# Performance work log

Hardware: AMD Instinct MI355X
Metric: run time of the kernel (lower is better)

## Reference

```python
import jax, jax.numpy as jnp
import numpy as np

N_DIMS = 8
MAPPING_DIMS = [0, 2, 4, 6]
COND_DIMS = [1, 3, 5, 7]
N_BINS = 32
MIN_BIN_W = 1e-3
MIN_BIN_H = 1e-3
MIN_DERIV = 1e-3
PI = np.pi
N = 524288


def _gather(v, idx):
    # v: (..., K[+1]), idx: (...) -> (...)
    return jnp.take_along_axis(v, idx[..., None], axis=-1)[..., 0]


def circular_quadratic_spline(x, uw, uh, ud, inverse):
    """Circular rational-quadratic spline on [-pi, pi] (Durkan et al. / Rezende et al.).
    x: (N, M); uw, uh, ud: (N, M, K)."""
    K = uw.shape[-1]
    left, right, bottom, top = -PI, PI, -PI, PI
    # circular boundary: derivative at right edge == derivative at left edge
    ud = jnp.concatenate([ud, ud[..., :1]], axis=-1)  # (N, M, K+1)

    widths = jax.nn.softmax(uw, axis=-1)
    widths = MIN_BIN_W + (1.0 - MIN_BIN_W * K) * widths
    cumw = jnp.pad(jnp.cumsum(widths, axis=-1), [(0, 0), (0, 0), (1, 0)])
    cumw = left + (right - left) * cumw
    cumw = cumw.at[..., 0].set(left).at[..., -1].set(right)
    widths = cumw[..., 1:] - cumw[..., :-1]

    derivatives = MIN_DERIV + jax.nn.softplus(ud)

    heights = jax.nn.softmax(uh, axis=-1)
    heights = MIN_BIN_H + (1.0 - MIN_BIN_H * K) * heights
    cumh = jnp.pad(jnp.cumsum(heights, axis=-1), [(0, 0), (0, 0), (1, 0)])
    cumh = bottom + (top - bottom) * cumh
    cumh = cumh.at[..., 0].set(bottom).at[..., -1].set(top)
    heights = cumh[..., 1:] - cumh[..., :-1]

    # per-element bin search (searchsorted via comparison-sum)
    bins = cumh if inverse else cumw
    idx = jnp.clip(jnp.sum(x[..., None] >= bins, axis=-1) - 1, 0, K - 1)

    in_cumw = _gather(cumw, idx)
    in_w = _gather(widths, idx)
    in_cumh = _gather(cumh, idx)
    in_delta = _gather(heights / widths, idx)
    d0 = _gather(derivatives, idx)
    d1 = _gather(derivatives, idx + 1)
    in_h = _gather(heights, idx)

    if inverse:
        dy = x - in_cumh
        s = d0 + d1 - 2.0 * in_delta
        a = dy * s + in_h * (in_delta - d0)
        b = in_h * d0 - dy * s
        c_ = -in_delta * dy
        disc = b * b - 4.0 * a * c_
        root = (2.0 * c_) / (-b - jnp.sqrt(disc))
        out = root * in_w + in_cumw
        t1m = root * (1.0 - root)
        denom = in_delta + s * t1m
        dnum = in_delta ** 2 * (d1 * root ** 2 + 2.0 * in_delta * t1m + d0 * (1.0 - root) ** 2)
        logabsdet = -(jnp.log(dnum) - 2.0 * jnp.log(denom))
        return out, logabsdet
    theta = (x - in_cumw) / in_w
    t1m = theta * (1.0 - theta)
    s = d0 + d1 - 2.0 * in_delta
    denom = in_delta + s * t1m
    num = in_h * (in_delta * theta ** 2 + d0 * t1m)
    out = in_cumh + num / denom
    dnum = in_delta ** 2 * (d1 * theta ** 2 + 2.0 * in_delta * t1m + d0 * (1.0 - theta) ** 2)
    logabsdet = jnp.log(dnum) - 2.0 * jnp.log(denom)
    return out, logabsdet


def setup_inputs() -> dict:
    key = jax.random.key(0)
    ks = jax.random.split(key, 8)
    x = jax.random.uniform(ks[0], (N, N_DIMS), jnp.float32, minval=-PI, maxval=PI)
    c = jax.random.normal(ks[1], (N, 128), jnp.float32)
    W1 = jax.random.normal(ks[2], (256, 140), jnp.float32) * (140 ** -0.5)
    b1 = jax.random.normal(ks[3], (256,), jnp.float32) * 0.01
    W2 = jax.random.normal(ks[4], (256, 256), jnp.float32) * (256 ** -0.5)
    b2 = jax.random.normal(ks[5], (256,), jnp.float32) * 0.01
    W3 = jax.random.normal(ks[6], (384, 256), jnp.float32) * (256 ** -0.5)
    b3 = jax.random.normal(ks[7], (384,), jnp.float32) * 0.01
    return {"x": x, "c": c, "W1": W1, "b1": b1, "W2": W2, "b2": b2,
            "W3": W3, "b3": b3, "inverse": 0}


def reference(x, c, W1, b1, W2, b2, W3, b3, inverse):
    m_idx = jnp.array(MAPPING_DIMS)
    c_idx = jnp.array(COND_DIMS)
    x_map = x[..., m_idx]          # (N, 4)
    x_cond = x[..., c_idx]         # (N, 4)
    inp = jnp.concatenate([x_cond, jnp.sin(x_cond), jnp.cos(x_cond), c], axis=-1)
    h = jax.nn.leaky_relu(inp @ W1.T + b1, negative_slope=0.01)
    h = jax.nn.leaky_relu(h @ W2.T + b2, negative_slope=0.01)
    outs = (h @ W3.T + b3).reshape(x.shape[0], len(MAPPING_DIMS), N_BINS, 3)
    w, hh, d = outs[..., 0], outs[..., 1], outs[..., 2]
    y_map, logabsdet = circular_quadratic_spline(x_map, w, hh, d, bool(inverse))
    y_unsort = jnp.concatenate([y_map, x_cond], axis=-1)
    perm = [0] * N_DIMS
    for i, j in enumerate(MAPPING_DIMS + COND_DIMS):
        perm[j] = i
    y = y_unsort[..., jnp.array(perm)]
    return y, logabsdet.sum(axis=-1)
```

## Files before the change

kernel.cpp:

```cpp
#include <hip/hip_runtime.h>
#include <math.h>

#define NROWS_TOTAL 524288
#define BR 64
#define NTH 512
#define PI_F 3.14159265358979323846f
#define TWO_PI_F 6.28318530717958647692f

typedef float f32x4 __attribute__((ext_vector_type(4)));
typedef _Float16 half8 __attribute__((ext_vector_type(8)));
typedef _Float16 half4v __attribute__((ext_vector_type(4)));

#define OFF_A 0
#define OFF_B 67584
#define LDS_BYTES 135168
#define PITCH_ACT 528
#define PITCH_OUT 1540
#define OFF_LAD 100352

#define W1_OFF 0
#define W2_OFF 40960
#define W3_OFF 106496
#define WHI_TOT 204800

struct h2 { _Float16 hi, lo; };
__device__ __forceinline__ h2 split16(float v){
  h2 r;
  r.hi = (_Float16)v;
  r.lo = (_Float16)(v - (float)r.hi);
  return r;
}

template<int NK, int NCT, bool RELU, bool OUTF32>
__device__ __forceinline__ void gemm_phase(unsigned char* LDS,
    const _Float16* __restrict__ WH, const _Float16* __restrict__ WL,
    const float* __restrict__ bias,
    int srcOff, int dstOff, int wave, int lrow, int lhi)
{
  constexpr int NS = NK / 32;
  f32x4 acc[4][NCT];
  #pragma unroll
  for (int rg = 0; rg < 4; rg++)
    #pragma unroll
    for (int ct = 0; ct < NCT; ct++)
      acc[rg][ct] = (f32x4){0.f, 0.f, 0.f, 0.f};

  const int ko = lhi * 8;
  #pragma unroll
  for (int ksl = 0; ksl < NS; ksl++){
    half8 ah[4], al[4];
    #pragma unroll
    for (int rg = 0; rg < 4; rg++){
      const unsigned char* p = LDS + srcOff + (rg * 16 + lrow) * PITCH_ACT
                               + (ksl * 32 + ko) * 2;
      ah[rg] = *(const half8*)p;
      al[rg] = *(const half8*)(p + 64 * PITCH_ACT);
    }
    #pragma unroll
    for (int ct = 0; ct < NCT; ct++){
      const int o = (wave * NCT + ct) * 16 + lrow;
      const size_t woff = (size_t)o * NK + ksl * 32 + ko;
      half8 wh = *(const half8*)(WH + woff);
      half8 wl = *(const half8*)(WL + woff);
      #pragma unroll
      for (int rg = 0; rg < 4; rg++){
        acc[rg][ct] = __builtin_amdgcn_mfma_f32_16x16x32_f16(ah[rg], wh, acc[rg][ct], 0, 0, 0);
        acc[rg][ct] = __builtin_amdgcn_mfma_f32_16x16x32_f16(al[rg], wh, acc[rg][ct], 0, 0, 0);
        acc[rg][ct] = __builtin_amdgcn_mfma_f32_16x16x32_f16(ah[rg], wl, acc[rg][ct], 0, 0, 0);
      }
    }
  }
  __syncthreads();
  #pragma unroll
  for (int ct = 0; ct < NCT; ct++){
    const int col = (wave * NCT + ct) * 16 + lrow;
    const float bv = bias[col];
    #pragma unroll
    for (int rg = 0; rg < 4; rg++){
      #pragma unroll
      for (int j = 0; j < 4; j++){
        float v = acc[rg][ct][j] + bv;
        if (RELU) v = (v >= 0.f) ? v : 0.01f * v;
        const int row = rg * 16 + lhi * 4 + j;
        if (OUTF32){
          *(float*)(LDS + (size_t)row * PITCH_OUT + col * 4) = v;
        } else {
          h2 s = split16(v);
          *(_Float16*)(LDS + dstOff + row * PITCH_ACT + col * 2) = s.hi;
          *(_Float16*)(LDS + dstOff + (row + 64) * PITCH_ACT + col * 2) = s.lo;
        }
      }
    }
  }
  __syncthreads();
}

__global__ void wconv_kernel(const float* __restrict__ W1, const float* __restrict__ W2,
                             const float* __restrict__ W3, _Float16* __restrict__ wb)
{
  int i = blockIdx.x * 256 + threadIdx.x;
  float v;
  if (i < 40960){
    int o = i / 160, k = i - o * 160;
    v = (k < 140) ? W1[o * 140 + k] : 0.f;
  } else if (i < 106496){
    v = W2[i - 40960];
  } else {
    v = W3[i - 106496];
  }
  h2 s = split16(v);
  wb[i] = s.hi;
  wb[i + WHI_TOT] = s.lo;
}

__global__ __launch_bounds__(NTH, 2) void spline_fused(
    const float* __restrict__ x, const float* __restrict__ c,
    const float* __restrict__ b1, const float* __restrict__ b2,
    const float* __restrict__ b3, const _Float16* __restrict__ wb,
    const int* __restrict__ invp, float* __restrict__ out)
{
  __shared__ __align__(16) unsigned char LDS[LDS_BYTES];
  const int tid  = threadIdx.x;
  const int wave = tid >> 6;
  const int lane = tid & 63;
  const int lrow = lane & 15;
  const int lhi  = lane >> 4;
  const int row0 = blockIdx.x * BR;

  {
    const float4* c4 = (const float4*)(c + (size_t)row0 * 128);
    #pragma unroll
    for (int i = 0; i < 4; i++){
      int q = tid + i * NTH;
      float4 v = c4[q];
      int r = q >> 5, cg = (q & 31) * 4 + 12;
      h2 s0 = split16(v.x), s1 = split16(v.y), s2 = split16(v.z), s3 = split16(v.w);
      half4v hv = {s0.hi, s1.hi, s2.hi, s3.hi};
      half4v lv = {s0.lo, s1.lo, s2.lo, s3.lo};
      *(half4v*)(LDS + OFF_B + r * PITCH_ACT + cg * 2) = hv;
      *(half4v*)(LDS + OFF_B + (r + 64) * PITCH_ACT + cg * 2) = lv;
    }
    if (tid < BR){
      int n = row0 + tid;
      float4 xa = *(const float4*)(x + (size_t)n * 8);
      float4 xb = *(const float4*)(x + (size_t)n * 8 + 4);
      float xc0 = xa.y, xc1 = xa.w, xc2 = xb.y, xc3 = xb.w;
      float f[12] = {xc0, xc1, xc2, xc3,
                     sinf(xc0), sinf(xc1), sinf(xc2), sinf(xc3),
                     cosf(xc0), cosf(xc1), cosf(xc2), cosf(xc3)};
      unsigned char* rp = LDS + OFF_B + tid * PITCH_ACT;
      #pragma unroll
      for (int g = 0; g < 3; g++){
        h2 s0 = split16(f[4*g+0]), s1 = split16(f[4*g+1]);
        h2 s2 = split16(f[4*g+2]), s3 = split16(f[4*g+3]);
        half4v hv = {s0.hi, s1.hi, s2.hi, s3.hi};
        half4v lv = {s0.lo, s1.lo, s2.lo, s3.lo};
        *(half4v*)(rp + g * 8) = hv;
        *(half4v*)(rp + 64 * PITCH_ACT + g * 8) = lv;
      }
      #pragma unroll
      for (int z = 0; z < 5; z++){
        *(unsigned long long*)(rp + 280 + z * 8) = 0ull;
        *(unsigned long long*)(rp + 64 * PITCH_ACT + 280 + z * 8) = 0ull;
      }
    }
  }
  __syncthreads();

  const _Float16* WLO = wb + WHI_TOT;
  gemm_phase<160, 2, true , false>(LDS, wb + W1_OFF, WLO + W1_OFF, b1, OFF_B, OFF_A, wave, lrow, lhi);
  gemm_phase<256, 2, true , false>(LDS, wb + W2_OFF, WLO + W2_OFF, b2, OFF_A, OFF_B, wave, lrow, lhi);
  gemm_phase<256, 3, false, true >(LDS, wb + W3_OFF, WLO + W3_OFF, b3, OFF_B, 0,     wave, lrow, lhi);

  if (tid < 256){
    const int r = tid & 63;
    const int d = tid >> 6;
    const int n = row0 + r;
    const int inv = invp[0];

    const float* ob = (const float*)(LDS + (size_t)r * PITCH_OUT) + d * 96;

    float wn[32], hn[32];
    float mw = ob[0], mh = ob[1];
    #pragma unroll
    for (int b = 1; b < 32; b++){
      mw = fmaxf(mw, ob[3*b]);
      mh = fmaxf(mh, ob[3*b + 1]);
    }
    float sw = 0.f, sh = 0.f;
    #pragma unroll
    for (int b = 0; b < 32; b++){
      float ew = expf(ob[3*b] - mw);     wn[b] = ew; sw += ew;
      float eh = expf(ob[3*b + 1] - mh); hn[b] = eh; sh += eh;
    }
    const float C1 = 1.0f - 32.0f * 1e-3f;
    float iw = C1 / sw, ih = C1 / sh;
    #pragma unroll
    for (int b = 0; b < 32; b++){
      wn[b] = 1e-3f + wn[b] * iw;
      hn[b] = 1e-3f + hn[b] * ih;
    }

    float2 xv = *(const float2*)(x + (size_t)n * 8 + 2 * d);
    float xm = xv.x, xcv = xv.y;

    bool fnd = false; int idx = 31;
    float cw = -PI_F, loA = 0.f, szA = 0.f;
    #pragma unroll
    for (int b = 0; b < 31; b++){
      float wbv = TWO_PI_F * (inv ? hn[b] : wn[b]);
      float reb = cw + wbv;
      if (!fnd && xm < reb){ fnd = true; idx = b; loA = cw; szA = wbv; }
      cw = reb;
    }
    if (!fnd){ loA = cw; szA = PI_F - cw; }

    float ch = -PI_F, loB = 0.f, szB = 0.f;
    #pragma unroll
    for (int b = 0; b < 31; b++){
      float hbv = TWO_PI_F * (inv ? wn[b] : hn[b]);
      if (b == idx){ loB = ch; szB = hbv; }
      ch += hbv;
    }
    if (idx == 31){ loB = ch; szB = PI_F - ch; }

    float le, wbw, lh, hb;
    if (inv){ lh = loA; hb = szA; le = loB; wbw = szB; }
    else    { le = loA; wbw = szA; lh = loB; hb = szB; }

    int i2 = (idx + 1) & 31;
    float ud0 = ob[idx * 3 + 2];
    float ud1 = ob[i2  * 3 + 2];
    auto softplus = [](float v) -> float {
      return fmaxf(v, 0.f) + log1pf(expf(-fabsf(v)));
    };
    float d0 = 1e-3f + softplus(ud0);
    float d1 = 1e-3f + softplus(ud1);

    float delta = hb / wbw;
    float outv, lad;
    if (inv){
      float dy = xm - lh;
      float s  = d0 + d1 - 2.f * delta;
      float aq = dy * s + hb * (delta - d0);
      float bq = hb * d0 - dy * s;
      float cq = -delta * dy;
      float disc = bq * bq - 4.f * aq * cq;
      float root = (2.f * cq) / (-bq - sqrtf(disc));
      outv = root * wbw + le;
      float t1m = root * (1.f - root);
      float denom = delta + s * t1m;
      float dnum = delta * delta * (d1 * root * root + 2.f * delta * t1m + d0 * (1.f - root) * (1.f - root));
      lad = -(logf(dnum) - 2.f * logf(denom));
    } else {
      float theta = (xm - le) / wbw;
      float t1m = theta * (1.f - theta);
      float s   = d0 + d1 - 2.f * delta;
      float denom = delta + s * t1m;
      float num = hb * (delta * theta * theta + d0 * t1m);
      outv = lh + num / denom;
      float dnum = delta * delta * (d1 * theta * theta + 2.f * delta * t1m + d0 * (1.f - theta) * (1.f - theta));
      lad = logf(dnum) - 2.f * logf(denom);
    }

    out[(size_t)n * 8 + 2 * d]     = outv;
    out[(size_t)n * 8 + 2 * d + 1] = xcv;
    *(float*)(LDS + OFF_LAD + (r * 4 + d) * 4) = lad;
  }
  __syncthreads();
  if (tid < BR){
    const float* lp = (const float*)(LDS + OFF_LAD);
    float sld = lp[tid * 4] + lp[tid * 4 + 1] + lp[tid * 4 + 2] + lp[tid * 4 + 3];
    out[(size_t)NROWS_TOTAL * 8 + row0 + tid] = sld;
  }
}

extern "C" void kernel_launch(void* const* d_in, const int* in_sizes, int n_in,
                              void* d_out, int out_size, void* d_ws, size_t ws_size,
                              hipStream_t stream)
{
  (void)in_sizes; (void)n_in; (void)out_size; (void)ws_size;
  const float* x  = (const float*)d_in[0];
  const float* c  = (const float*)d_in[1];
  const float* W1 = (const float*)d_in[2];
  const float* b1 = (const float*)d_in[3];
  const float* W2 = (const float*)d_in[4];
  const float* b2 = (const float*)d_in[5];
  const float* W3 = (const float*)d_in[6];
  const float* b3 = (const float*)d_in[7];
  const int*  inv = (const int*)d_in[8];
  _Float16* wb = (_Float16*)d_ws;
  float* out = (float*)d_out;

  hipLaunchKernelGGL(wconv_kernel, dim3(800), dim3(256), 0, stream, W1, W2, W3, wb);
  hipLaunchKernelGGL(spline_fused, dim3(NROWS_TOTAL / BR), dim3(NTH), 0, stream,
                     x, c, b1, b2, b3, wb, inv, out);
}
```

Before: 1.300 ms.

## Shrink LDS to a single activation buffer and split spline epilogue for higher occupancy

The kernel now keeps one in-place activation buffer, holding GEMM results in registers across a barrier before overwriting it, which halves LDS use. The f32 logits are staged in two 32-row halves so they fit, and the spline runs on 128 threads per half. Launch bounds rise to 4 blocks per CU to exploit the smaller footprint, and weight fragments are double-buffered across k-slices to hide global load latency. Risks include register pressure under the tighter occupancy bound, extra barriers, and a spline stage with less parallelism per half.

```diff
diff --git a/kernel.cpp b/kernel.cpp
--- a/kernel.cpp
+++ b/kernel.cpp
@@ -11,12 +11,10 @@
 typedef _Float16 half8 __attribute__((ext_vector_type(8)));
 typedef _Float16 half4v __attribute__((ext_vector_type(4)));
 
-#define OFF_A 0
-#define OFF_B 67584
-#define LDS_BYTES 135168
 #define PITCH_ACT 528
 #define PITCH_OUT 1540
-#define OFF_LAD 100352
+#define OFF_LAD 67584
+#define LDS_BYTES 68608
 
 #define W1_OFF 0
 #define W2_OFF 40960
@@ -31,14 +29,13 @@
   return r;
 }
 
-template<int NK, int NCT, bool RELU, bool OUTF32>
-__device__ __forceinline__ void gemm_phase(unsigned char* LDS,
+template<int NK, int NCT>
+__device__ __forceinline__ void gemm_core(const unsigned char* LDS,
+    f32x4 (&acc)[4][NCT],
     const _Float16* __restrict__ WH, const _Float16* __restrict__ WL,
-    const float* __restrict__ bias,
-    int srcOff, int dstOff, int wave, int lrow, int lhi)
+    int wave, int lrow, int lhi)
 {
   constexpr int NS = NK / 32;
-  f32x4 acc[4][NCT];
   #pragma unroll
   for (int rg = 0; rg < 4; rg++)
     #pragma unroll
@@ -46,31 +43,44 @@
       acc[rg][ct] = (f32x4){0.f, 0.f, 0.f, 0.f};
 
   const int ko = lhi * 8;
+  half8 whb[2][NCT], wlb[2][NCT];
+  #pragma unroll
+  for (int ct = 0; ct < NCT; ct++){
+    const int o = (wave * NCT + ct) * 16 + lrow;
+    whb[0][ct] = *(const half8*)(WH + (size_t)o * NK + ko);
+    wlb[0][ct] = *(const half8*)(WL + (size_t)o * NK + ko);
+  }
   #pragma unroll
   for (int ksl = 0; ksl < NS; ksl++){
-    half8 ah[4], al[4];
+    const int cur = ksl & 1, nxt = cur ^ 1;
+    if (ksl + 1 < NS){
+      #pragma unroll
+      for (int ct = 0; ct < NCT; ct++){
+        const int o = (wave * NCT + ct) * 16 + lrow;
+        const size_t woff = (size_t)o * NK + (ksl + 1) * 32 + ko;
+        whb[nxt][ct] = *(const half8*)(WH + woff);
+        wlb[nxt][ct] = *(const half8*)(WL + woff);
+      }
+    }
     #pragma unroll
     for (int rg = 0; rg < 4; rg++){
-      const unsigned char* p = LDS + srcOff + (rg * 16 + lrow) * PITCH_ACT
-                               + (ksl * 32 + ko) * 2;
-      ah[rg] = *(const half8*)p;
-      al[rg] = *(const half8*)(p + 64 * PITCH_ACT);
-    }
-    #pragma unroll
-    for (int ct = 0; ct < NCT; ct++){
-      const int o = (wave * NCT + ct) * 16 + lrow;
-      const size_t woff = (size_t)o * NK + ksl * 32 + ko;
-      half8 wh = *(const half8*)(WH + woff);
-      half8 wl = *(const half8*)(WL + woff);
-      #pragma unroll
-      for (int rg = 0; rg < 4; rg++){
-        acc[rg][ct] = __builtin_amdgcn_mfma_f32_16x16x32_f16(ah[rg], wh, acc[rg][ct], 0, 0, 0);
-        acc[rg][ct] = __builtin_amdgcn_mfma_f32_16x16x32_f16(al[rg], wh, acc[rg][ct], 0, 0, 0);
-        acc[rg][ct] = __builtin_amdgcn_mfma_f32_16x16x32_f16(ah[rg], wl, acc[rg][ct], 0, 0, 0);
-      }
-    }
-  }
-  __syncthreads();
+      const unsigned char* p = LDS + (rg * 16 + lrow) * PITCH_ACT + (ksl * 32 + ko) * 2;
+      half8 ah = *(const half8*)p;
+      half8 al = *(const half8*)(p + 64 * PITCH_ACT);
+      #pragma unroll
+      for (int ct = 0; ct < NCT; ct++){
+        acc[rg][ct] = __builtin_amdgcn_mfma_f32_16x16x32_f16(ah, whb[cur][ct], acc[rg][ct], 0, 0, 0);
+        acc[rg][ct] = __builtin_amdgcn_mfma_f32_16x16x32_f16(al, whb[cur][ct], acc[rg][ct], 0, 0, 0);
+        acc[rg][ct] = __builtin_amdgcn_mfma_f32_16x16x32_f16(ah, wlb[cur][ct], acc[rg][ct], 0, 0, 0);
+      }
+    }
+  }
+}
+
+template<int NCT>
+__device__ __forceinline__ void epi_f16(unsigned char* LDS, f32x4 (&acc)[4][NCT],
+    const float* __restrict__ bias, int wave, int lrow, int lhi)
+{
   #pragma unroll
   for (int ct = 0; ct < NCT; ct++){
     const int col = (wave * NCT + ct) * 16 + lrow;
@@ -80,19 +90,133 @@
       #pragma unroll
       for (int j = 0; j < 4; j++){
         float v = acc[rg][ct][j] + bv;
-        if (RELU) v = (v >= 0.f) ? v : 0.01f * v;
+        v = (v >= 0.f) ? v : 0.01f * v;
         const int row = rg * 16 + lhi * 4 + j;
-        if (OUTF32){
-          *(float*)(LDS + (size_t)row * PITCH_OUT + col * 4) = v;
-        } else {
-          h2 s = split16(v);
-          *(_Float16*)(LDS + dstOff + row * PITCH_ACT + col * 2) = s.hi;
-          *(_Float16*)(LDS + dstOff + (row + 64) * PITCH_ACT + col * 2) = s.lo;
-        }
-      }
-    }
-  }
-  __syncthreads();
+        h2 s = split16(v);
+        *(_Float16*)(LDS + row * PITCH_ACT + col * 2) = s.hi;
+        *(_Float16*)(LDS + (row + 64) * PITCH_ACT + col * 2) = s.lo;
+      }
+    }
+  }
+}
+
+template<int NCT>
+__device__ __forceinline__ void epi_logits(unsigned char* LDS, f32x4 (&acc)[4][NCT],
+    const float* __restrict__ bias, int rgBase, int wave, int lrow, int lhi)
+{
+  #pragma unroll
+  for (int ct = 0; ct < NCT; ct++){
+    const int col = (wave * NCT + ct) * 16 + lrow;
+    const float bv = bias[col];
+    #pragma unroll
+    for (int rg = 0; rg < 2; rg++){
+      #pragma unroll
+      for (int j = 0; j < 4; j++){
+        const int rowl = rg * 16 + lhi * 4 + j;
+        *(float*)(LDS + (size_t)rowl * PITCH_OUT + col * 4)
+            = acc[rgBase + rg][ct][j] + bv;
+      }
+    }
+  }
+}
+
+__device__ __forceinline__ void spline_half(unsigned char* LDS, int half, int tid,
+    int row0, const float* __restrict__ x, int inv, float* __restrict__ out)
+{
+  if (tid >= 128) return;
+  const int lr = tid & 31;
+  const int d  = tid >> 5;
+  const int r  = half * 32 + lr;
+  const int n  = row0 + r;
+
+  const float* ob = (const float*)(LDS + (size_t)lr * PITCH_OUT) + d * 96;
+
+  float wn[32], hn[32];
+  float mw = ob[0], mh = ob[1];
+  #pragma unroll
+  for (int b = 1; b < 32; b++){
+    mw = fmaxf(mw, ob[3*b]);
+    mh = fmaxf(mh, ob[3*b + 1]);
+  }
+  float sw = 0.f, sh = 0.f;
+  #pragma unroll
+  for (int b = 0; b < 32; b++){
+    float ew = expf(ob[3*b] - mw);     wn[b] = ew; sw += ew;
+    float eh = expf(ob[3*b + 1] - mh); hn[b] = eh; sh += eh;
+  }
+  const float C1 = 1.0f - 32.0f * 1e-3f;
+  float iw = C1 / sw, ih = C1 / sh;
+  #pragma unroll
+  for (int b = 0; b < 32; b++){
+    wn[b] = 1e-3f + wn[b] * iw;
+    hn[b] = 1e-3f + hn[b] * ih;
+  }
+
+  float2 xv = *(const float2*)(x + (size_t)n * 8 + 2 * d);
+  float xm = xv.x, xcv = xv.y;
+
+  bool fnd = false; int idx = 31;
+  float cw = -PI_F, loA = 0.f, szA = 0.f;
+  #pragma unroll
+  for (int b = 0; b < 31; b++){
+    float wbv = TWO_PI_F * (inv ? hn[b] : wn[b]);
+    float reb = cw + wbv;
+    if (!fnd && xm < reb){ fnd = true; idx = b; loA = cw; szA = wbv; }
+    cw = reb;
+  }
+  if (!fnd){ loA = cw; szA = PI_F - cw; }
+
+  float ch = -PI_F, loB = 0.f, szB = 0.f;
+  #pragma unroll
+  for (int b = 0; b < 31; b++){
+    float hbv = TWO_PI_F * (inv ? wn[b] : hn[b]);
+    if (b == idx){ loB = ch; szB = hbv; }
+    ch += hbv;
+  }
+  if (idx == 31){ loB = ch; szB = PI_F - ch; }
+
+  float le, wbw, lh, hb;
+  if (inv){ lh = loA; hb = szA; le = loB; wbw = szB; }
+  else    { le = loA; wbw = szA; lh = loB; hb = szB; }
+
+  int i2 = (idx + 1) & 31;
+  float ud0 = ob[idx * 3 + 2];
+  float ud1 = ob[i2  * 3 + 2];
+  auto softplus = [](float v) -> float {
+    return fmaxf(v, 0.f) + log1pf(expf(-fabsf(v)));
+  };
+  float d0 = 1e-3f + softplus(ud0);
+  float d1 = 1e-3f + softplus(ud1);
+
+  float delta = hb / wbw;
+  float outv, lad;
+  if (inv){
+    float dy = xm - lh;
+    float s  = d0 + d1 - 2.f * delta;
+    float aq = dy * s + hb * (delta - d0);
+    float bq = hb * d0 - dy * s;
+    float cq = -delta * dy;
+    float disc = bq * bq - 4.f * aq * cq;
+    float root = (2.f * cq) / (-bq - sqrtf(disc));
+    outv = root * wbw + le;
+    float t1m = root * (1.f - root);
+    float denom = delta + s * t1m;
+    float dnum = delta * delta * (d1 * root * root + 2.f * delta * t1m + d0 * (1.f - root) * (1.f - root));
+    lad = -(logf(dnum) - 2.f * logf(denom));
+  } else {
+    float theta = (xm - le) / wbw;
+    float t1m = theta * (1.f - theta);
+    float s   = d0 + d1 - 2.f * delta;
+    float denom = delta + s * t1m;
+    float num = hb * (delta * theta * theta + d0 * t1m);
+    outv = lh + num / denom;
+    float dnum = delta * delta * (d1 * theta * theta + 2.f * delta * t1m + d0 * (1.f - theta) * (1.f - theta));
+    lad = logf(dnum) - 2.f * logf(denom);
+  }
+
+  out[(size_t)n * 8 + 2 * d]     = outv;
+  out[(size_t)n * 8 + 2 * d + 1] = xcv;
+  *(float*)(LDS + OFF_LAD + (r * 4 + d) * 4) = lad;
 }
 
 __global__ void wconv_kernel(const float* __restrict__ W1, const float* __restrict__ W2,
@@ -113,7 +237,7 @@
   wb[i + WHI_TOT] = s.lo;
 }
 
-__global__ __launch_bounds__(NTH, 2) void spline_fused(
+__global__ __launch_bounds__(NTH, 4) void spline_fused(
     const float* __restrict__ x, const float* __restrict__ c,
     const float* __restrict__ b1, const float* __restrict__ b2,
     const float* __restrict__ b3, const _Float16* __restrict__ wb,
@@ -137,8 +261,8 @@
       h2 s0 = split16(v.x), s1 = split16(v.y), s2 = split16(v.z), s3 = split16(v.w);
       half4v hv = {s0.hi, s1.hi, s2.hi, s3.hi};
       half4v lv = {s0.lo, s1.lo, s2.lo, s3.lo};
-      *(half4v*)(LDS + OFF_B + r * PITCH_ACT + cg * 2) = hv;
-      *(half4v*)(LDS + OFF_B + (r + 64) * PITCH_ACT + cg * 2) = lv;
+      *(half4v*)(LDS + r * PITCH_ACT + cg * 2) = hv;
+      *(half4v*)(LDS + (r + 64) * PITCH_ACT + cg * 2) = lv;
     }
     if (tid < BR){
       int n = row0 + tid;
@@ -148,7 +272,7 @@
       float f[12] = {xc0, xc1, xc2, xc3,
                      sinf(xc0), sinf(xc1), sinf(xc2), sinf(xc3),
                      cosf(xc0), cosf(xc1), cosf(xc2), cosf(xc3)};
-      unsigned char* rp = LDS + OFF_B + tid * PITCH_ACT;
+      unsigned char* rp = LDS + tid * PITCH_ACT;
       #pragma unroll
       for (int g = 0; g < 3; g++){
         h2 s0 = split16(f[4*g+0]), s1 = split16(f[4*g+1]);
@@ -168,110 +292,38 @@
   __syncthreads();
 
   const _Float16* WLO = wb + WHI_TOT;
-  gemm_phase<160, 2, true , false>(LDS, wb + W1_OFF, WLO + W1_OFF, b1, OFF_B, OFF_A, wave, lrow, lhi);
-  gemm_phase<256, 2, true , false>(LDS, wb + W2_OFF, WLO + W2_OFF, b2, OFF_A, OFF_B, wave, lrow, lhi);
-  gemm_phase<256, 3, false, true >(LDS, wb + W3_OFF, WLO + W3_OFF, b3, OFF_B, 0,     wave, lrow, lhi);
-
-  if (tid < 256){
-    const int r = tid & 63;
-    const int d = tid >> 6;
-    const int n = row0 + r;
-    const int inv = invp[0];
-
-    const float* ob = (const float*)(LDS + (size_t)r * PITCH_OUT) + d * 96;
-
-    float wn[32], hn[32];
-    float mw = ob[0], mh = ob[1];
-    #pragma unroll
-    for (int b = 1; b < 32; b++){
-      mw = fmaxf(mw, ob[3*b]);
-      mh = fmaxf(mh, ob[3*b + 1]);
-    }
-    float sw = 0.f, sh = 0.f;
-    #pragma unroll
-    for (int b = 0; b < 32; b++){
-      float ew = expf(ob[3*b] - mw);     wn[b] = ew; sw += ew;
-      float eh = expf(ob[3*b + 1] - mh); hn[b] = eh; sh += eh;
-    }
-    const float C1 = 1.0f - 32.0f * 1e-3f;
-    float iw = C1 / sw, ih = C1 / sh;
-    #pragma unroll
-    for (int b = 0; b < 32; b++){
-      wn[b] = 1e-3f + wn[b] * iw;
-      hn[b] = 1e-3f + hn[b] * ih;
-    }
-
-    float2 xv = *(const float2*)(x + (size_t)n * 8 + 2 * d);
-    float xm = xv.x, xcv = xv.y;
-
-    bool fnd = false; int idx = 31;
-    float cw = -PI_F, loA = 0.f, szA = 0.f;
-    #pragma unroll
-    for (int b = 0; b < 31; b++){
-      float wbv = TWO_PI_F * (inv ? hn[b] : wn[b]);
-      float reb = cw + wbv;
-      if (!fnd && xm < reb){ fnd = true; idx = b; loA = cw; szA = wbv; }
-      cw = reb;
-    }
-    if (!fnd){ loA = cw; szA = PI_F - cw; }
-
-    float ch = -PI_F, loB = 0.f, szB = 0.f;
-    #pragma unroll
-    for (int b = 0; b < 31; b++){
-      float hbv = TWO_PI_F * (inv ? wn[b] : hn[b]);
-      if (b == idx){ loB = ch; szB = hbv; }
-      ch += hbv;
-    }
-    if (idx == 31){ loB = ch; szB = PI_F - ch; }
-
-    float le, wbw, lh, hb;
-    if (inv){ lh = loA; hb = szA; le = loB; wbw = szB; }
-    else    { le = loA; wbw = szA; lh = loB; hb = szB; }
-
-    int i2 = (idx + 1) & 31;
-    float ud0 = ob[idx * 3 + 2];
-    float ud1 = ob[i2  * 3 + 2];
-    auto softplus = [](float v) -> float {
-      return fmaxf(v, 0.f) + log1pf(expf(-fabsf(v)));
-    };
-    float d0 = 1e-3f + softplus(ud0);
-    float d1 = 1e-3f + softplus(ud1);
-
-    float delta = hb / wbw;
-    float outv, lad;
-    if (inv){
-      float dy = xm - lh;
-      float s  = d0 + d1 - 2.f * delta;
-      float aq = dy * s + hb * (delta - d0);
-      float bq = hb * d0 - dy * s;
-      float cq = -delta * dy;
-      float disc = bq * bq - 4.f * aq * cq;
-      float root = (2.f * cq) / (-bq - sqrtf(disc));
-      outv = root * wbw + le;
-      float t1m = root * (1.f - root);
-      float denom = delta + s * t1m;
-      float dnum = delta * delta * (d1 * root * root + 2.f * delta * t1m + d0 * (1.f - root) * (1.f - root));
-      lad = -(logf(dnum) - 2.f * logf(denom));
-    } else {
-      float theta = (xm - le) / wbw;
-      float t1m = theta * (1.f - theta);
-      float s   = d0 + d1 - 2.f * delta;
-      float denom = delta + s * t1m;
-      float num = hb * (delta * theta * theta + d0 * t1m);
-      outv = lh + num / denom;
-      float dnum = delta * delta * (d1 * theta * theta + 2.f * delta * t1m + d0 * (1.f - theta) * (1.f - theta));
-      lad = logf(dnum) - 2.f * logf(denom);
-    }
-
-    out[(size_t)n * 8 + 2 * d]     = outv;
-    out[(size_t)n * 8 + 2 * d + 1] = xcv;
-    *(float*)(LDS + OFF_LAD + (r * 4 + d) * 4) = lad;
+  const int inv = invp[0];
+
+  {
+    f32x4 acc[4][2];
+    gemm_core<160, 2>(LDS, acc, wb + W1_OFF, WLO + W1_OFF, wave, lrow, lhi);
+    __syncthreads();
+    epi_f16<2>(LDS, acc, b1, wave, lrow, lhi);
+  }
+  __syncthreads();
+  {
+    f32x4 acc[4][2];
+    gemm_core<256, 2>(LDS, acc, wb + W2_OFF, WLO + W2_OFF, wave, lrow, lhi);
+    __syncthreads();
+    epi_f16<2>(LDS, acc, b2, wave, lrow, lhi);
+  }
+  __syncthreads();
+  {
+    f32x4 acc[4][3];
+    gemm_core<256, 3>(LDS, acc, wb + W3_OFF, WLO + W3_OFF, wave, lrow, lhi);
+    __syncthreads();
+    epi_logits<3>(LDS, acc, b3, 0, wave, lrow, lhi);
+    __syncthreads();
+    spline_half(LDS, 0, tid, row0, x, inv, out);
+    __syncthreads();
+    epi_logits<3>(LDS, acc, b3, 2, wave, lrow, lhi);
+    __syncthreads();
+    spline_half(LDS, 1, tid, row0, x, inv, out);
   }
   __syncthreads();
   if (tid < BR){
-    const float* lp = (const float*)(LDS + OFF_LAD);
-    float sld = lp[tid * 4] + lp[tid * 4 + 1] + lp[tid * 4 + 2] + lp[tid * 4 + 3];
-    out[(size_t)NROWS_TOTAL * 8 + row0 + tid] = sld;
+    float4 v = *(const float4*)(LDS + OFF_LAD + tid * 16);
+    out[(size_t)NROWS_TOTAL * 8 + row0 + tid] = v.x + v.y + v.z + v.w;
   }
 }
 
```

New measurement: 1.098 ms. -15.5%, faster.
